# Kernel optimization log

Measured on AMD Instinct MI355X. Metric: run time of the kernel, lower is better.

## Reference

```python
import jax, jax.numpy as jnp
import numpy as np
from jax import lax

D = 300          # embedding dim (data.x.shape[1])
H = 1024         # hidden_state_dim
H2 = H // 2
V_SENSES = 25000   # last_idx_senses
V_GLOBALS = 50000  # last_idx_globals - last_idx_senses
NUM_NODES = 80000
T = 1024           # seq_len (batch=1)


def _lin_init(k, out_f, in_f):
    # torch.nn.Linear default: U(-1/sqrt(in), 1/sqrt(in)) for W and b
    kw, kb = jax.random.split(k)
    lim = 1.0 / np.sqrt(in_f)
    W = jax.random.uniform(kw, (out_f, in_f), jnp.float32, -lim, lim)
    b = jax.random.uniform(kb, (out_f,), jnp.float32, -lim, lim)
    return W, b


def setup_inputs() -> dict:
    key = jax.random.key(0)
    ks = jax.random.split(key, 6)
    X = jax.random.normal(ks[0], (NUM_NODES, D), jnp.float32) * 0.1
    W1, b1 = _lin_init(ks[1], H, D + H)
    W2, b2 = _lin_init(ks[2], H2, H + H2)
    Wg, bg = _lin_init(ks[3], V_GLOBALS, H2)
    Ws, bs = _lin_init(ks[4], V_SENSES, H2)
    indices = jax.random.randint(ks[5], (1, T), 0, NUM_NODES, jnp.int32)
    return {"X": X, "W1": W1, "b1": b1, "W2": W2, "b2": b2,
            "Wg": Wg, "bg": bg, "Ws": Ws, "bs": bs, "indices": indices}


def reference(X, W1, b1, W2, b2, Wg, bg, Ws, bs, indices):
    # Sequential RNN over flattened (batch, seq) steps; memory_h1/h2 start at
    # zeros and carry across all steps (as the in-place .data.copy_ does).
    # Dropout is treated as identity (eval mode).
    idx = indices.reshape(-1)  # [T]

    def step(carry, i):
        h1, h2 = carry  # [H], [H2]
        e = X[i]  # gather current-word embedding, [D]
        h1n = jax.nn.leaky_relu(
            jnp.dot(W1, jnp.concatenate([e, h1])) + b1, negative_slope=0.01)
        h2n = jax.nn.leaky_relu(
            jnp.dot(W2, jnp.concatenate([h1n, h2])) + b2, negative_slope=0.01)
        return (h1n, h2n), h2n

    init = (jnp.zeros((H,), X.dtype), jnp.zeros((H2,), X.dtype))
    _, h2s = lax.scan(step, init, idx)  # h2s: [T, H2]

    # Output projections batched over all timesteps (same math as per-step).
    logp_globals = jax.nn.log_softmax(h2s @ Wg.T + bg, axis=-1)  # [T, V_GLOBALS]
    logp_senses = jax.nn.log_softmax(h2s @ Ws.T + bs, axis=-1)   # [T, V_SENSES]
    return logp_globals, logp_senses
```

## Files before the change

kernel.cpp:

```cpp
#include <hip/hip_runtime.h>
#include <hip/hip_bf16.h>
#include <stdint.h>

#define T_STEPS 1024
#define NH1 1024
#define NH2 512
#define D_IN 300
#define W1_LD 1324
#define W2_LD 1536
#define NVG 50000
#define NVS 25000
#define NTILE_G 391
#define NTILE_S 196
#define TPL (NTILE_G + NTILE_S)
#define NTILE (4 * TPL)

typedef unsigned long long u64;
typedef __bf16 bf16x8 __attribute__((ext_vector_type(8)));
typedef short s16x8 __attribute__((ext_vector_type(8)));
typedef float f32x4 __attribute__((ext_vector_type(4)));

__global__ __launch_bounds__(256) void e_kernel(
    const float* __restrict__ X,
    const float* __restrict__ W1,
    const float* __restrict__ b1,
    const int* __restrict__ idx,
    float* __restrict__ E,
    unsigned* __restrict__ ctl)
{
  if (blockIdx.x == 0 && threadIdx.x < 16) ctl[threadIdx.x] = 0u;

  __shared__ float Xs[32 * 300];
  const int rb = blockIdx.x & 7;
  const int tb = blockIdx.x >> 3;
  const int r0 = rb * 128;
  const int t0 = tb * 32;

  for (int t = 0; t < 32; ++t) {
    int node = idx[t0 + t];
    for (int c = threadIdx.x; c < 300; c += 256)
      Xs[t * 300 + c] = X[(size_t)node * D_IN + c];
  }
  __syncthreads();

  const int rl = threadIdx.x & 127;
  const int th = threadIdx.x >> 7;
  const int tbase = th * 16;
  const int r = r0 + rl;

  float acc[16];
  const float bias = b1[r];
#pragma unroll
  for (int tt = 0; tt < 16; ++tt) acc[tt] = bias;

  const float* wrow = W1 + (size_t)r * W1_LD;
  for (int c0 = 0; c0 < 300; c0 += 4) {
    float w0 = wrow[c0 + 0];
    float w1 = wrow[c0 + 1];
    float w2 = wrow[c0 + 2];
    float w3 = wrow[c0 + 3];
#pragma unroll
    for (int tt = 0; tt < 16; ++tt) {
      const float* xr = Xs + (tbase + tt) * 300 + c0;
      acc[tt] += w0 * xr[0] + w1 * xr[1] + w2 * xr[2] + w3 * xr[3];
    }
  }
#pragma unroll
  for (int tt = 0; tt < 16; ++tt)
    E[(size_t)(t0 + tbase + tt) * NH1 + r] = acc[tt];
}

__global__ __launch_bounds__(512, 2) void rnn_kernel(
    const float* __restrict__ W1,
    const float* __restrict__ W2,
    const float* __restrict__ b2,
    const float* __restrict__ E,
    u64* __restrict__ buf1,
    u64* __restrict__ buf2,
    __hip_bfloat16* __restrict__ h2s,
    unsigned* __restrict__ ctl,
    const float* __restrict__ Wg,
    const float* __restrict__ bg,
    const float* __restrict__ Ws,
    const float* __restrict__ bs,
    float* __restrict__ out)
{
  __shared__ float lds1[2][NH1];
  __shared__ float lds2[2][NH2];
  __shared__ short As[256 * 64];
  __shared__ short Bs[128 * 64];
  __shared__ int s_role;
  __shared__ unsigned s_tile;

  if (threadIdx.x == 0) {
    int xcd;
    asm volatile("s_getreg_b32 %0, hwreg(HW_REG_XCC_ID)" : "=s"(xcd));
    xcd &= 7;
    unsigned rk = atomicAdd(&ctl[xcd], 1u);
    unsigned wnr;
    while ((wnr = __hip_atomic_load(&ctl[8], __ATOMIC_RELAXED,
                                    __HIP_MEMORY_SCOPE_AGENT)) == 0u) {
      if (rk == 31u) {
        atomicCAS(&ctl[8], 0u, (unsigned)(xcd + 1));
      } else {
        __builtin_amdgcn_s_sleep(16);
      }
    }
    int role;
    if (wnr == (unsigned)(xcd + 1))
      role = (rk < 32u) ? (int)rk : -2;
    else
      role = -1;
    s_role = role;
  }
  __syncthreads();
  const int role = s_role;
  if (role == -2) return;

  const int tid = threadIdx.x;
  const int lane = tid & 63;

  if (role >= 0) {
    const int b = role;
    const int w = tid >> 6;
    const int wvid = b * 8 + w;
    const int r1 = wvid * 4;
    const int r2 = wvid * 2;
    const int oct = (w + b) & 7;

    float w1r[4][16];
#pragma unroll
    for (int i = 0; i < 4; ++i)
#pragma unroll
      for (int j = 0; j < 16; ++j)
        w1r[i][j] = W1[(size_t)(r1 + i) * W1_LD + D_IN + lane + 64 * j];

    float w2r[2][24];
#pragma unroll
    for (int i = 0; i < 2; ++i)
#pragma unroll
      for (int j = 0; j < 24; ++j)
        w2r[i][j] = W2[(size_t)(r2 + i) * W2_LD + lane + 64 * j];

    const float b2a = b2[r2];
    const float b2b = b2[r2 + 1];

    for (int s = 0; s <= T_STEPS; ++s) {
      float ev = 0.f;
      if (s < T_STEPS) ev = E[(size_t)s * NH1 + r1 + (lane & 3)];

      float v1[2] = {0.f, 0.f};
      float v2 = 0.f;
      unsigned miss = 0;
      if (s >= 1) miss |= 0x3u;
      if (s >= 2) miss |= 0x4u;
      const u64* p1 = buf1 + (size_t)(s & 3) * NH1 + 128 * oct + lane;
      const u64* p2 = buf2 + (size_t)((s - 1) & 3) * NH2 + 64 * oct + lane;
      const unsigned tag1 = (unsigned)s;
      const unsigned tag2 = (unsigned)(s - 1);

      while (miss) {
        u64 t1[2], t2;
        asm volatile(
            "global_load_dwordx2 %0, %3, off sc0 sc1\n\t"
            "global_load_dwordx2 %1, %3, off offset:512 sc0 sc1\n\t"
            "global_load_dwordx2 %2, %4, off sc0 sc1\n\t"
            "s_waitcnt vmcnt(0)"
            : "=&v"(t1[0]), "=&v"(t1[1]), "=&v"(t2)
            : "v"(p1), "v"(p2)
            : "memory");
#pragma unroll
        for (int j = 0; j < 2; ++j)
          if ((miss & (1u << j)) && (unsigned)(t1[j] >> 32) == tag1) {
            v1[j] = __uint_as_float((unsigned)t1[j]);
            miss &= ~(1u << j);
          }
        if ((miss & 0x4u) && (unsigned)(t2 >> 32) == tag2) {
          v2 = __uint_as_float((unsigned)t2);
          miss &= ~0x4u;
        }
      }

      const int pb = s & 1;
#pragma unroll
      for (int j = 0; j < 2; ++j) lds1[pb][128 * oct + 64 * j + lane] = v1[j];
      lds2[pb][64 * oct + lane] = v2;
      __syncthreads();

      float a0 = 0.f, a1 = 0.f, a2 = 0.f, a3 = 0.f, a4 = 0.f, a5 = 0.f;
#pragma unroll
      for (int j = 0; j < 16; ++j) {
        float h = lds1[pb][lane + 64 * j];
        a0 += w1r[0][j] * h;
        a1 += w1r[1][j] * h;
        a2 += w1r[2][j] * h;
        a3 += w1r[3][j] * h;
        a4 += w2r[0][j] * h;
        a5 += w2r[1][j] * h;
      }
#pragma unroll
      for (int j = 0; j < 8; ++j) {
        float h = lds2[pb][lane + 64 * j];
        a4 += w2r[0][16 + j] * h;
        a5 += w2r[1][16 + j] * h;
      }

#pragma unroll
      for (int off = 32; off; off >>= 1) {
        a0 += __shfl_xor(a0, off);
        a1 += __shfl_xor(a1, off);
        a2 += __shfl_xor(a2, off);
        a3 += __shfl_xor(a3, off);
      }
      if (s < T_STEPS && lane < 4) {
        float x = (lane == 0 ? a0 : lane == 1 ? a1 : lane == 2 ? a2 : a3) + ev;
        float h = x > 0.f ? x : 0.01f * x;
        u64 pk = ((u64)(unsigned)(s + 1) << 32) | (u64)__float_as_uint(h);
        u64* dst = buf1 + (size_t)((s + 1) & 3) * NH1 + r1 + lane;
        asm volatile("global_store_dwordx2 %0, %1, off sc0"
                     :: "v"(dst), "v"(pk) : "memory");
      }

      if (s >= 1) {
#pragma unroll
        for (int off = 32; off; off >>= 1) {
          a4 += __shfl_xor(a4, off);
          a5 += __shfl_xor(a5, off);
        }
        if (lane >= 4 && lane < 6) {
          int i = lane - 4;
          float x = (i == 0 ? a4 : a5) + (i == 0 ? b2a : b2b);
          float h = x > 0.f ? x : 0.01f * x;
          u64 pk = ((u64)(unsigned)s << 32) | (u64)__float_as_uint(h);
          u64* dst = buf2 + (size_t)(s & 3) * NH2 + r2 + i;
          asm volatile("global_store_dwordx2 %0, %1, off sc0"
                       :: "v"(dst), "v"(pk) : "memory");
          h2s[(size_t)(s - 1) * NH2 + r2 + i] = __float2bfloat16(h);
        }
      }
    }

    asm volatile("s_waitcnt vmcnt(0)" ::: "memory");
    if (lane >= 4 && lane < 6) {
      u64 pk = (u64)2048u << 32;
      u64* dst = buf2 + r2 + (lane - 4);
      asm volatile("global_store_dwordx2 %0, %1, off sc0"
                   :: "v"(dst), "v"(pk) : "memory");
    }
    return;
  }

  {
    const int wv = tid >> 6;
    const int wm = (wv & 1) * 128;
    const int wn = (wv >> 1) * 32;
    const int ml = lane & 15;
    const int kq = lane >> 4;
    const int arow = tid >> 3;
    const int kc = tid & 7;
    const int phys = kc ^ (arow & 7);

    for (;;) {
      if (tid == 0) s_tile = atomicAdd(&ctl[9], 1u);
      __syncthreads();
      const unsigned t = s_tile;
      if (t >= (unsigned)NTILE) break;
      const int lvl = (int)(t / (unsigned)TPL);
      const int rem = (int)(t - (unsigned)lvl * (unsigned)TPL);
      const int seg = rem >= NTILE_G;
      const int nb = seg ? rem - NTILE_G : rem;
      const int m0 = lvl * 256;
      const int n0 = nb * 128;
      const int N = seg ? NVS : NVG;
      const float* B = seg ? Ws : Wg;
      const float* bias = seg ? bs : bg;
      float* C = seg ? out + (size_t)1024 * NVG : out;

      const unsigned need = (lvl == 3) ? 2048u : (unsigned)(256 * (lvl + 1) + 4);
      {
        const u64* gp = buf2 + tid;
        for (;;) {
          u64 v;
          asm volatile("global_load_dwordx2 %0, %1, off sc0 sc1\n\t"
                       "s_waitcnt vmcnt(0)"
                       : "=v"(v) : "v"(gp) : "memory");
          unsigned tg = (unsigned)(v >> 32);
          if (tg >= need && tg <= 2048u) break;
          __builtin_amdgcn_s_sleep(64);
        }
      }
      __syncthreads();

      f32x4 acc[8][2];
#pragma unroll
      for (int i = 0; i < 8; ++i)
#pragma unroll
        for (int j = 0; j < 2; ++j)
          acc[i][j] = (f32x4){0.f, 0.f, 0.f, 0.f};

      for (int kb = 0; kb < 512; kb += 64) {
        __syncthreads();
        const short* ab = (const short*)h2s + (size_t)(m0 + arow) * 512 + kb + kc * 8;
        s16x8 av0, av1, av2, av3;
        asm volatile(
            "global_load_dwordx4 %0, %4, off sc0 sc1\n\t"
            "global_load_dwordx4 %1, %5, off sc0 sc1\n\t"
            "global_load_dwordx4 %2, %6, off sc0 sc1\n\t"
            "global_load_dwordx4 %3, %7, off sc0 sc1"
            : "=&v"(av0), "=&v"(av1), "=&v"(av2), "=&v"(av3)
            : "v"(ab), "v"(ab + 32768), "v"(ab + 65536), "v"(ab + 98304)
            : "memory");
        int gr0 = n0 + arow;       if (gr0 >= N) gr0 = N - 1;
        int gr1 = n0 + 64 + arow;  if (gr1 >= N) gr1 = N - 1;
        const float* bp0 = B + (size_t)gr0 * 512 + kb + kc * 8;
        const float* bp1 = B + (size_t)gr1 * 512 + kb + kc * 8;
        f32x4 f00 = ((const f32x4*)bp0)[0], f01 = ((const f32x4*)bp0)[1];
        f32x4 f10 = ((const f32x4*)bp1)[0], f11 = ((const f32x4*)bp1)[1];
        bf16x8 bv0, bv1;
        bv0[0] = (__bf16)f00[0]; bv0[1] = (__bf16)f00[1];
        bv0[2] = (__bf16)f00[2]; bv0[3] = (__bf16)f00[3];
        bv0[4] = (__bf16)f01[0]; bv0[5] = (__bf16)f01[1];
        bv0[6] = (__bf16)f01[2]; bv0[7] = (__bf16)f01[3];
        bv1[0] = (__bf16)f10[0]; bv1[1] = (__bf16)f10[1];
        bv1[2] = (__bf16)f10[2]; bv1[3] = (__bf16)f10[3];
        bv1[4] = (__bf16)f11[0]; bv1[5] = (__bf16)f11[1];
        bv1[6] = (__bf16)f11[2]; bv1[7] = (__bf16)f11[3];
        asm volatile("s_waitcnt vmcnt(0)" ::: "memory");
        *(s16x8*)(As + (arow +   0) * 64 + phys * 8) = av0;
        *(s16x8*)(As + (arow +  64) * 64 + phys * 8) = av1;
        *(s16x8*)(As + (arow + 128) * 64 + phys * 8) = av2;
        *(s16x8*)(As + (arow + 192) * 64 + phys * 8) = av3;
        *(bf16x8*)(Bs + (arow +  0) * 64 + phys * 8) = bv0;
        *(bf16x8*)(Bs + (arow + 64) * 64 + phys * 8) = bv1;
        __syncthreads();
#pragma unroll
        for (int ks = 0; ks < 2; ++ks) {
          bf16x8 af[8], bfr[2];
#pragma unroll
          for (int i = 0; i < 8; ++i) {
            int row = wm + 16 * i + ml;
            int pk2 = (ks * 4 + kq) ^ (row & 7);
            af[i] = *(const bf16x8*)(As + row * 64 + pk2 * 8);
          }
#pragma unroll
          for (int j = 0; j < 2; ++j) {
            int row = wn + 16 * j + ml;
            int pk2 = (ks * 4 + kq) ^ (row & 7);
            bfr[j] = *(const bf16x8*)(Bs + row * 64 + pk2 * 8);
          }
#pragma unroll
          for (int i = 0; i < 8; ++i)
#pragma unroll
            for (int j = 0; j < 2; ++j)
              acc[i][j] = __builtin_amdgcn_mfma_f32_16x16x32_bf16(
                  af[i], bfr[j], acc[i][j], 0, 0, 0);
        }
      }

      float bvv[2];
#pragma unroll
      for (int j = 0; j < 2; ++j) {
        int n = n0 + wn + 16 * j + ml;
        bvv[j] = (n < N) ? bias[n] : 0.f;
      }
#pragma unroll
      for (int i = 0; i < 8; ++i) {
        int mrow = m0 + wm + 16 * i + kq * 4;
#pragma unroll
        for (int j = 0; j < 2; ++j) {
          int n = n0 + wn + 16 * j + ml;
          if (n < N) {
#pragma unroll
            for (int r = 0; r < 4; ++r)
              C[(size_t)(mrow + r) * N + n] = acc[i][j][r] + bvv[j];
          }
        }
      }
    }
  }
}

__global__ __launch_bounds__(512) void norm_kernel(float* __restrict__ out)
{
  const int b = blockIdx.x;
  const int t = b & 1023;
  const int seg = b >> 10;
  const size_t base = seg == 0 ? (size_t)t * NVG
                               : (size_t)1024 * NVG + (size_t)t * NVS;
  const int len4 = (seg == 0 ? NVG : NVS) >> 2;
  f32x4* p = (f32x4*)(out + base);
  const int lane = threadIdx.x & 63;
  const int wv = threadIdx.x >> 6;
  __shared__ float redm[8], reds[8];

  float m = -3.0e38f, ssum = 0.f;
  for (int i = threadIdx.x; i < len4; i += 512) {
    f32x4 v = p[i];
    float vm = fmaxf(fmaxf(v[0], v[1]), fmaxf(v[2], v[3]));
    if (vm > m) { ssum *= expf(m - vm); m = vm; }
    ssum += expf(v[0] - m) + expf(v[1] - m) + expf(v[2] - m) + expf(v[3] - m);
  }
#pragma unroll
  for (int off = 32; off; off >>= 1) {
    float mo = __shfl_xor(m, off);
    float so = __shfl_xor(ssum, off);
    float mn = fmaxf(m, mo);
    ssum = ssum * expf(m - mn) + so * expf(mo - mn);
    m = mn;
  }
  if (lane == 0) { redm[wv] = m; reds[wv] = ssum; }
  __syncthreads();
  float M = redm[0], S = reds[0];
#pragma unroll
  for (int k = 1; k < 8; ++k) {
    float mo = redm[k], so = reds[k];
    float mn = fmaxf(M, mo);
    S = S * expf(M - mn) + so * expf(mo - mn);
    M = mn;
  }
  const float lse = M + logf(S);

  for (int i = threadIdx.x; i < len4; i += 512) {
    f32x4 v = p[i];
    v[0] -= lse; v[1] -= lse; v[2] -= lse; v[3] -= lse;
    p[i] = v;
  }
}

extern "C" void kernel_launch(void* const* d_in, const int* in_sizes, int n_in,
                              void* d_out, int out_size, void* d_ws, size_t ws_size,
                              hipStream_t stream) {
  const float* X  = (const float*)d_in[0];
  const float* W1 = (const float*)d_in[1];
  const float* b1 = (const float*)d_in[2];
  const float* W2 = (const float*)d_in[3];
  const float* b2 = (const float*)d_in[4];
  const float* Wg = (const float*)d_in[5];
  const float* bg = (const float*)d_in[6];
  const float* Ws = (const float*)d_in[7];
  const float* bs = (const float*)d_in[8];
  const int* idx = (const int*)d_in[9];
  float* out = (float*)d_out;

  char* ws = (char*)d_ws;
  float* E = (float*)ws;
  __hip_bfloat16* h2s = (__hip_bfloat16*)(ws + (size_t)4194304);
  u64* buf1 = (u64*)(ws + (size_t)5242880);
  u64* buf2 = (u64*)(ws + (size_t)5275648);
  unsigned* ctl = (unsigned*)(out + (size_t)1024 * (NVG + NVS) - 16);

  e_kernel<<<256, 256, 0, stream>>>(X, W1, b1, idx, E, ctl);
  rnn_kernel<<<512, 512, 0, stream>>>(W1, W2, b2, E, buf1, buf2, h2s, ctl,
                                      Wg, bg, Ws, bs, out);
  norm_kernel<<<2048, 512, 0, stream>>>(out);
}
```

Before: 2.852 ms.

## Streamline projection-tile readiness waits and write h2s through to coherent memory

The GEMM tile workers now wait on the RNN progress flags only once per level. For levels below 3 a single thread polls one flag, and for the final level one wavefront checks all flags. The h2s stores switch to system-coherent short stores, which lets the A-operand loads become ordinary cached vector loads with no forced waitcnt. The flag buffers are zeroed at the start of each run. This reduces polling traffic and load latency in the projection phase, but correctness now depends on the coherence and ordering assumptions behind checking a single flag.

New measurement: 3.288 ms. +15.3%, slower.

```diff
diff --git a/kernel.cpp b/kernel.cpp
--- a/kernel.cpp
+++ b/kernel.cpp
@@ -26,9 +26,13 @@
     const float* __restrict__ b1,
     const int* __restrict__ idx,
     float* __restrict__ E,
-    unsigned* __restrict__ ctl)
+    unsigned* __restrict__ ctl,
+    u64* __restrict__ bufz)
 {
-  if (blockIdx.x == 0 && threadIdx.x < 16) ctl[threadIdx.x] = 0u;
+  if (blockIdx.x == 0) {
+    for (int i = threadIdx.x; i < 6144; i += 256) bufz[i] = 0ull;
+    if (threadIdx.x < 16) ctl[threadIdx.x] = 0u;
+  }
 
   __shared__ float Xs[32 * 300];
   const int rb = blockIdx.x & 7;
@@ -235,7 +239,12 @@
           u64* dst = buf2 + (size_t)(s & 3) * NH2 + r2 + i;
           asm volatile("global_store_dwordx2 %0, %1, off sc0"
                        :: "v"(dst), "v"(pk) : "memory");
-          h2s[(size_t)(s - 1) * NH2 + r2 + i] = __float2bfloat16(h);
+          __hip_bfloat16 hb = __float2bfloat16(h);
+          unsigned hv = (unsigned)*reinterpret_cast<unsigned short*>(&hb);
+          unsigned short* hdst =
+              (unsigned short*)h2s + (size_t)(s - 1) * NH2 + r2 + i;
+          asm volatile("global_store_short %0, %1, off sc0 sc1"
+                       :: "v"(hdst), "v"(hv) : "memory");
         }
       }
     }
@@ -259,6 +268,7 @@
     const int arow = tid >> 3;
     const int kc = tid & 7;
     const int phys = kc ^ (arow & 7);
+    int done_lvl = -1;
 
     for (;;) {
       if (tid == 0) s_tile = atomicAdd(&ctl[9], 1u);
@@ -276,20 +286,41 @@
       const float* bias = seg ? bs : bg;
       float* C = seg ? out + (size_t)1024 * NVG : out;
 
-      const unsigned need = (lvl == 3) ? 2048u : (unsigned)(256 * (lvl + 1) + 4);
-      {
-        const u64* gp = buf2 + tid;
-        for (;;) {
-          u64 v;
-          asm volatile("global_load_dwordx2 %0, %1, off sc0 sc1\n\t"
-                       "s_waitcnt vmcnt(0)"
-                       : "=v"(v) : "v"(gp) : "memory");
-          unsigned tg = (unsigned)(v >> 32);
-          if (tg >= need && tg <= 2048u) break;
-          __builtin_amdgcn_s_sleep(64);
-        }
-      }
-      __syncthreads();
+      if (lvl > done_lvl) {
+        if (lvl < 3) {
+          if (tid == 0) {
+            const unsigned need = (unsigned)(256 * (lvl + 1) + 4);
+            for (;;) {
+              u64 v;
+              asm volatile("global_load_dwordx2 %0, %1, off sc0 sc1\n\t"
+                           "s_waitcnt vmcnt(0)"
+                           : "=v"(v) : "v"(buf2) : "memory");
+              unsigned tg = (unsigned)(v >> 32);
+              if (tg >= need && tg <= 2048u) break;
+              __builtin_amdgcn_s_sleep(32);
+            }
+          }
+        } else {
+          if (tid < 64) {
+            for (;;) {
+              int ok = 1;
+#pragma unroll
+              for (int j = 0; j < 8; ++j) {
+                u64 v;
+                const u64* gp = buf2 + lane + 64 * j;
+                asm volatile("global_load_dwordx2 %0, %1, off sc0 sc1\n\t"
+                             "s_waitcnt vmcnt(0)"
+                             : "=v"(v) : "v"(gp) : "memory");
+                if ((unsigned)(v >> 32) != 2048u) ok = 0;
+              }
+              if (__all(ok)) break;
+              __builtin_amdgcn_s_sleep(32);
+            }
+          }
+        }
+        __syncthreads();
+        done_lvl = lvl;
+      }
 
       f32x4 acc[8][2];
 #pragma unroll
@@ -301,15 +332,10 @@
       for (int kb = 0; kb < 512; kb += 64) {
         __syncthreads();
         const short* ab = (const short*)h2s + (size_t)(m0 + arow) * 512 + kb + kc * 8;
-        s16x8 av0, av1, av2, av3;
-        asm volatile(
-            "global_load_dwordx4 %0, %4, off sc0 sc1\n\t"
-            "global_load_dwordx4 %1, %5, off sc0 sc1\n\t"
-            "global_load_dwordx4 %2, %6, off sc0 sc1\n\t"
-            "global_load_dwordx4 %3, %7, off sc0 sc1"
-            : "=&v"(av0), "=&v"(av1), "=&v"(av2), "=&v"(av3)
-            : "v"(ab), "v"(ab + 32768), "v"(ab + 65536), "v"(ab + 98304)
-            : "memory");
+        s16x8 av0 = *(const s16x8*)(ab);
+        s16x8 av1 = *(const s16x8*)(ab + 32768);
+        s16x8 av2 = *(const s16x8*)(ab + 65536);
+        s16x8 av3 = *(const s16x8*)(ab + 98304);
         int gr0 = n0 + arow;       if (gr0 >= N) gr0 = N - 1;
         int gr1 = n0 + 64 + arow;  if (gr1 >= N) gr1 = N - 1;
         const float* bp0 = B + (size_t)gr0 * 512 + kb + kc * 8;
@@ -325,7 +351,6 @@
         bv1[2] = (__bf16)f10[2]; bv1[3] = (__bf16)f10[3];
         bv1[4] = (__bf16)f11[0]; bv1[5] = (__bf16)f11[1];
         bv1[6] = (__bf16)f11[2]; bv1[7] = (__bf16)f11[3];
-        asm volatile("s_waitcnt vmcnt(0)" ::: "memory");
         *(s16x8*)(As + (arow +   0) * 64 + phys * 8) = av0;
         *(s16x8*)(As + (arow +  64) * 64 + phys * 8) = av1;
         *(s16x8*)(As + (arow + 128) * 64 + phys * 8) = av2;
@@ -449,7 +474,7 @@
   u64* buf2 = (u64*)(ws + (size_t)5275648);
   unsigned* ctl = (unsigned*)(out + (size_t)1024 * (NVG + NVS) - 16);
 
-  e_kernel<<<256, 256, 0, stream>>>(X, W1, b1, idx, E, ctl);
+  e_kernel<<<256, 256, 0, stream>>>(X, W1, b1, idx, E, ctl, buf1);
   rnn_kernel<<<512, 512, 0, stream>>>(W1, W2, b2, E, buf1, buf2, h2s, ctl,
                                       Wg, bg, Ws, bs, out);
   norm_kernel<<<2048, 512, 0, stream>>>(out);
```
